# Performance work log

Measured on AMD Instinct MI355X. Metric: run time of the kernel, lower is better.

## Reference

```python
import jax, jax.numpy as jnp
import numpy as np

B, L, V = 4, 1024, 1280
N_EMBD, N_BIN, N_HID = 768, 8, 32
HORIZON = 10.0


def setup_inputs() -> dict:
    key = jax.random.key(0)
    k_h, k_age, k_gap, k_tgt, k_w1, k_w2 = jax.random.split(key, 6)
    h = jax.random.normal(k_h, (B, L, N_EMBD), dtype=jnp.float32)
    # ages increase along a trajectory; gaps in [0, 2) years
    age = jnp.sort(jax.random.uniform(k_age, (B, L), dtype=jnp.float32) * 80.0, axis=-1)
    targets_age = age + jax.random.uniform(k_gap, (B, L), dtype=jnp.float32) * 2.0
    delta_t = targets_age - age  # passed to forward but unused (as in torch source)
    targets = jax.random.randint(k_tgt, (B, L), 0, V, dtype=jnp.int32)
    W1 = jax.random.normal(k_w1, (N_EMBD, N_BIN * N_HID), dtype=jnp.float32) * 0.02
    W2 = jax.random.normal(k_w2, (N_HID, V), dtype=jnp.float32) * 0.02
    return {"h": h, "age": age, "targets_age": targets_age, "delta_t": delta_t,
            "targets": targets, "W1": W1, "W2": W2}


def _time_to_event(age, targets_age, targets):
    # delta_full[b,i,j] = targets_age[b,j] - age[b,i]
    delta_full = targets_age[:, None, :] - age[:, :, None]  # (B,L,L)
    i_idx = jnp.arange(L)
    # torch.triu(diagonal=0): keep targets[b,j] where j>=i, else 0
    upper = (i_idx[None, :] >= i_idx[:, None])  # (L,L) mask, col>=row
    targets_exp = jnp.where(upper[None, :, :], targets[:, None, :], 0)  # (B,L,L)
    # scatter-reduce amin of position index j into vocab slot targets_exp[b,i,j]
    # sentinel L plays the role of torch's -1 (min over srcs ignores it; src<=L-1)
    b_ix = jnp.arange(B)[:, None, None]
    r_ix = i_idx[None, :, None]
    src = jnp.broadcast_to(i_idx[None, None, :], (B, L, L)).astype(jnp.int32)
    token_index = jnp.full((B, L, V), L, dtype=jnp.int32)
    token_index = token_index.at[b_ix, r_ix, targets_exp].min(src)
    no_event = token_index == L
    token_index = jnp.where(no_event, L - 1, token_index)  # (B,L,V)
    tte = jnp.take_along_axis(delta_full, token_index, axis=-1)  # (B,L,V)
    return tte, no_event, token_index


def reference(h, age, targets_age, delta_t, targets, W1, W2):
    # two dense projections: (B,L,E) -> (B,L,n_bin,n_hid) -> (B,L,n_bin,V)
    x = jnp.einsum('ble,eo->blo', h, W1).reshape(B, L, N_BIN, N_HID)
    logits = jnp.einsum('blnh,hv->blnv', x, W2)
    tte, no_event, _ = _time_to_event(age, targets_age, targets)
    edges = jnp.linspace(0.0, HORIZON, N_BIN + 1)
    lo = edges[:-1][None, None, :, None]
    hi = edges[1:][None, None, :, None]
    t = tte[:, :, None, :]  # (B,L,1,V)
    censor_mask = ((t >= lo) & (t < hi)) | no_event[:, :, None, :]  # (B,L,n_bin,V)
    return logits, tte, censor_mask
```

## Files before the change

### kernel.cpp

```cpp
#include <hip/hip_runtime.h>
#include <hip/hip_bf16.h>

#define B_   4
#define L_   1024
#define V_   1280
#define NE_  768
#define NB_  8
#define NH_  32
#define NO_  (NB_*NH_)
#define BL_  (B_*L_)
#define M2_  (BL_*NB_)

typedef __attribute__((ext_vector_type(8))) short bf16x8;
typedef __attribute__((ext_vector_type(4))) float floatx4;

__device__ __forceinline__ unsigned short f2bf(float f) {
    unsigned int u = __float_as_uint(f);
    u += 0x7FFFu + ((u >> 16) & 1u);
    return (unsigned short)(u >> 16);
}

#define H4_N   (BL_*NE_/4)
#define W1T_N  (NO_*NE_)
#define W2T_N  (V_*NH_)
#define K0_TOT (H4_N + W1T_N + W2T_N)

__global__ __launch_bounds__(256) void k0_pack(const float* __restrict__ h,
                                               const float* __restrict__ W1,
                                               const float* __restrict__ W2,
                                               unsigned short* __restrict__ hb,
                                               unsigned short* __restrict__ W1T,
                                               unsigned short* __restrict__ W2T) {
    int id = blockIdx.x * 256 + threadIdx.x;
    if (id < H4_N) {
        float4 v = ((const float4*)h)[id];
        ushort4 o;
        o.x = f2bf(v.x); o.y = f2bf(v.y); o.z = f2bf(v.z); o.w = f2bf(v.w);
        ((ushort4*)hb)[id] = o;
    } else if (id < H4_N + W1T_N) {
        int j = id - H4_N;
        int o = j / NE_;
        int k = j - o * NE_;
        W1T[j] = f2bf(W1[(size_t)k * NO_ + o]);
    } else if (id < K0_TOT) {
        int j = id - H4_N - W1T_N;
        int v = j >> 5;
        int k = j & 31;
        W2T[j] = f2bf(W2[(size_t)k * V_ + v]);
    }
}

__global__ __launch_bounds__(256) void k1_gemm(const unsigned short* __restrict__ hb,
                                               const unsigned short* __restrict__ W1T,
                                               unsigned short* __restrict__ Xb) {
    __shared__ short A_lds[64][40];
    __shared__ short Bt_lds[64][40];

    const int t      = threadIdx.x;
    const int m0     = blockIdx.x * 64;
    const int n0     = blockIdx.y * 64;
    const int l      = t & 63;
    const int w      = t >> 6;
    const int lane15 = l & 15;
    const int quad   = l >> 4;

    const int srow = t >> 2;
    const int sq   = (t & 3) * 8;

    const unsigned short* aptr = hb  + (size_t)(m0 + srow) * NE_ + sq;
    const unsigned short* bptr = W1T + (size_t)(n0 + srow) * NE_ + sq;

    floatx4 acc[4];
#pragma unroll
    for (int i = 0; i < 4; ++i) acc[i] = (floatx4){0.f, 0.f, 0.f, 0.f};

    bf16x8 av = *(const bf16x8*)aptr;
    bf16x8 bv = *(const bf16x8*)bptr;

    for (int k0 = 0; k0 < NE_; k0 += 32) {
        __syncthreads();
        *(bf16x8*)&A_lds[srow][sq]  = av;
        *(bf16x8*)&Bt_lds[srow][sq] = bv;
        __syncthreads();
        if (k0 + 32 < NE_) {
            av = *(const bf16x8*)(aptr + k0 + 32);
            bv = *(const bf16x8*)(bptr + k0 + 32);
        }
        bf16x8 af = *(bf16x8*)&A_lds[w * 16 + lane15][quad * 8];
#pragma unroll
        for (int nt = 0; nt < 4; ++nt) {
            bf16x8 bf = *(bf16x8*)&Bt_lds[nt * 16 + lane15][quad * 8];
            acc[nt] = __builtin_amdgcn_mfma_f32_16x16x32_bf16(af, bf, acc[nt], 0, 0, 0);
        }
    }

    const int rbase = m0 + w * 16 + quad * 4;
#pragma unroll
    for (int nt = 0; nt < 4; ++nt)
#pragma unroll
        for (int r = 0; r < 4; ++r)
            Xb[(size_t)(rbase + r) * NO_ + n0 + nt * 16 + lane15] = f2bf(acc[nt][r]);
}

__global__ __launch_bounds__(256) void k2_logits(const unsigned short* __restrict__ Xb,
                                                 const unsigned short* __restrict__ W2T,
                                                 float* __restrict__ outL) {
    const int t      = threadIdx.x;
    const int m0     = blockIdx.x * 64;
    const int l      = t & 63;
    const int w      = t >> 6;
    const int lane15 = l & 15;
    const int quad   = l >> 4;

    const int m = m0 + w * 16 + lane15;
    const bf16x8 af = *(const bf16x8*)(Xb + (size_t)m * NH_ + quad * 8);

    const int rbase = m0 + w * 16 + quad * 4;

#pragma unroll 4
    for (int nt = 0; nt < V_ / 16; ++nt) {
        bf16x8 bf = *(const bf16x8*)(W2T + (size_t)(nt * 16 + lane15) * NH_ + quad * 8);
        floatx4 c = (floatx4){0.f, 0.f, 0.f, 0.f};
        c = __builtin_amdgcn_mfma_f32_16x16x32_bf16(af, bf, c, 0, 0, 0);
#pragma unroll
        for (int r = 0; r < 4; ++r)
            outL[(size_t)(rbase + r) * V_ + nt * 16 + lane15] = c[r];
    }
}

#define K3_S 32

__global__ __launch_bounds__(256) void k3_tte(const float* __restrict__ age,
                                              const float* __restrict__ tage,
                                              const int*   __restrict__ targets,
                                              float* __restrict__ outT,
                                              float* __restrict__ outM) {
    __shared__ int   tg[L_];
    __shared__ float ta[L_];
    __shared__ float ag[K3_S];

    const int t      = threadIdx.x;
    const int v      = blockIdx.x * 256 + t;
    const int istart = blockIdx.y * K3_S;
    const int iend   = istart + K3_S;
    const int b      = blockIdx.z;

    for (int j = t; j < L_; j += 256) {
        tg[j] = targets[(size_t)b * L_ + j];
        ta[j] = tage[(size_t)b * L_ + j];
    }
    if (t < K3_S) ag[t] = age[(size_t)b * L_ + istart + t];
    __syncthreads();

    int cur = L_;
    for (int i = L_ - 1; i >= istart; --i) {
        const int ti = tg[i];
        if (ti == v) cur = i;
        if (i < iend) {
            int idx = cur;
            if (v == 0 && i >= 1) idx = 0;
            const bool noev = (idx == L_);
            const int  ic   = noev ? (L_ - 1) : idx;
            const float tte = ta[ic] - ag[i - istart];

            outT[((size_t)(b * L_ + i)) * V_ + v] = tte;

            const size_t mb = ((size_t)(b * L_ + i)) * NB_ * V_ + v;
#pragma unroll
            for (int n = 0; n < NB_; ++n) {
                const float lo = n * 1.25f;
                const float hi = (n + 1) * 1.25f;
                const bool in_bin = (tte >= lo) && (tte < hi);
                outM[mb + (size_t)n * V_] = (in_bin || noev) ? 1.0f : 0.0f;
            }
        }
    }
}

extern "C" void kernel_launch(void* const* d_in, const int* in_sizes, int n_in,
                              void* d_out, int out_size, void* d_ws, size_t ws_size,
                              hipStream_t stream) {
    const float* h       = (const float*)d_in[0];
    const float* age     = (const float*)d_in[1];
    const float* tage    = (const float*)d_in[2];
    const int*   targets = (const int*)  d_in[4];
    const float* W1      = (const float*)d_in[5];
    const float* W2      = (const float*)d_in[6];

    float* out  = (float*)d_out;
    float* outL = out;
    float* outT = out + (size_t)BL_ * NB_ * V_;
    float* outM = outT + (size_t)BL_ * V_;

    char* ws = (char*)d_ws;
    unsigned short* hb  = (unsigned short*)(ws);
    unsigned short* W1T = (unsigned short*)(ws + 6291456);
    unsigned short* W2T = (unsigned short*)(ws + 6291456 + 393216);
    unsigned short* Xb  = (unsigned short*)(ws + 6291456 + 393216 + 81920);

    k0_pack  <<<(K0_TOT + 255) / 256, 256, 0, stream>>>(h, W1, W2, hb, W1T, W2T);
    k1_gemm  <<<dim3(BL_/64, NO_/64), 256, 0, stream>>>(hb, W1T, Xb);
    k2_logits<<<M2_/64, 256, 0, stream>>>(Xb, W2T, outL);
    k3_tte   <<<dim3(V_/256, L_/K3_S, B_), 256, 0, stream>>>(age, tage, targets, outT, outM);
}
```

Measured before the change: 423.1 us.

## Precompute per-chunk next-occurrence table and split logits kernel across vocab tiles

A new pass scans each batch's targets once per vocab slot and records the next occurrence at every 16-row chunk boundary. The output kernel can then start each chunk from that table instead of rescanning from the end of the sequence. This removes the quadratic backward scan that made the old tte kernel costly, and the output kernel now writes float4 vectors. The logits kernel also gains a second grid dimension over vocab tiles for more parallelism, at the cost of reloading the A fragment in each tile.

New measurement: 426.9 us. Within noise of the previous version (+0.9%).

```diff
diff --git a/kernel.cpp b/kernel.cpp
--- a/kernel.cpp
+++ b/kernel.cpp
@@ -10,6 +10,7 @@
 #define NO_  (NB_*NH_)
 #define BL_  (B_*L_)
 #define M2_  (BL_*NB_)
+#define NCH_ 64
 
 typedef __attribute__((ext_vector_type(8))) short bf16x8;
 typedef __attribute__((ext_vector_type(4))) float floatx4;
@@ -107,6 +108,7 @@
                                                  float* __restrict__ outL) {
     const int t      = threadIdx.x;
     const int m0     = blockIdx.x * 64;
+    const int nt0    = blockIdx.y * 16;
     const int l      = t & 63;
     const int w      = t >> 6;
     const int lane15 = l & 15;
@@ -118,7 +120,7 @@
     const int rbase = m0 + w * 16 + quad * 4;
 
 #pragma unroll 4
-    for (int nt = 0; nt < V_ / 16; ++nt) {
+    for (int nt = nt0; nt < nt0 + 16; ++nt) {
         bf16x8 bf = *(const bf16x8*)(W2T + (size_t)(nt * 16 + lane15) * NH_ + quad * 8);
         floatx4 c = (floatx4){0.f, 0.f, 0.f, 0.f};
         c = __builtin_amdgcn_mfma_f32_16x16x32_bf16(af, bf, c, 0, 0, 0);
@@ -128,51 +130,80 @@
     }
 }
 
-#define K3_S 32
-
-__global__ __launch_bounds__(256) void k3_tte(const float* __restrict__ age,
+__global__ __launch_bounds__(256) void k3a_nxt(const int* __restrict__ targets,
+                                               int* __restrict__ nxt) {
+    const int b = blockIdx.x;
+    const int v = blockIdx.y * 256 + threadIdx.x;
+    __shared__ int tg[L_];
+    for (int j = threadIdx.x; j < L_; j += 256) tg[j] = targets[(size_t)b * L_ + j];
+    __syncthreads();
+    int cur = L_;
+    for (int j = L_ - 1; j >= 0; --j) {
+        if ((j & 15) == 15)
+            nxt[((size_t)b * NCH_ + (j >> 4)) * V_ + v] = cur;
+        if (tg[j] == v) cur = j;
+    }
+}
+
+__global__ __launch_bounds__(64) void k3b_out(const float* __restrict__ age,
                                               const float* __restrict__ tage,
                                               const int*   __restrict__ targets,
+                                              const int*   __restrict__ nxt,
                                               float* __restrict__ outT,
                                               float* __restrict__ outM) {
-    __shared__ int   tg[L_];
     __shared__ float ta[L_];
-    __shared__ float ag[K3_S];
-
-    const int t      = threadIdx.x;
-    const int v      = blockIdx.x * 256 + t;
-    const int istart = blockIdx.y * K3_S;
-    const int iend   = istart + K3_S;
-    const int b      = blockIdx.z;
-
-    for (int j = t; j < L_; j += 256) {
-        tg[j] = targets[(size_t)b * L_ + j];
-        ta[j] = tage[(size_t)b * L_ + j];
-    }
-    if (t < K3_S) ag[t] = age[(size_t)b * L_ + istart + t];
+    __shared__ int   tgc[16];
+    __shared__ float agc[16];
+
+    const int t  = threadIdx.x;
+    const int vt = blockIdx.x;
+    const int c  = blockIdx.y;
+    const int b  = blockIdx.z;
+    const int v0 = vt * 256 + t * 4;
+
+    for (int j = t; j < L_; j += 64) ta[j] = tage[(size_t)b * L_ + j];
+    if (t < 16) {
+        tgc[t] = targets[(size_t)b * L_ + c * 16 + t];
+        agc[t] = age[(size_t)b * L_ + c * 16 + t];
+    }
     __syncthreads();
 
-    int cur = L_;
-    for (int i = L_ - 1; i >= istart; --i) {
-        const int ti = tg[i];
-        if (ti == v) cur = i;
-        if (i < iend) {
-            int idx = cur;
-            if (v == 0 && i >= 1) idx = 0;
-            const bool noev = (idx == L_);
-            const int  ic   = noev ? (L_ - 1) : idx;
-            const float tte = ta[ic] - ag[i - istart];
-
-            outT[((size_t)(b * L_ + i)) * V_ + v] = tte;
-
-            const size_t mb = ((size_t)(b * L_ + i)) * NB_ * V_ + v;
-#pragma unroll
-            for (int n = 0; n < NB_; ++n) {
-                const float lo = n * 1.25f;
-                const float hi = (n + 1) * 1.25f;
-                const bool in_bin = (tte >= lo) && (tte < hi);
-                outM[mb + (size_t)n * V_] = (in_bin || noev) ? 1.0f : 0.0f;
-            }
+    int4 cur = *(const int4*)&nxt[((size_t)b * NCH_ + c) * V_ + v0];
+
+    for (int ii = 15; ii >= 0; --ii) {
+        const int   i  = c * 16 + ii;
+        const int   ti = tgc[ii];
+        const float ai = agc[ii];
+
+        if (ti == v0 + 0) cur.x = i;
+        if (ti == v0 + 1) cur.y = i;
+        if (ti == v0 + 2) cur.z = i;
+        if (ti == v0 + 3) cur.w = i;
+
+        int ix = cur.x, iy = cur.y, iz = cur.z, iw = cur.w;
+        if (v0 == 0 && i >= 1) ix = 0;
+        const bool nex = (ix == L_), ney = (iy == L_), nez = (iz == L_), new_ = (iw == L_);
+
+        float4 tt;
+        tt.x = ta[nex ? L_ - 1 : ix] - ai;
+        tt.y = ta[ney ? L_ - 1 : iy] - ai;
+        tt.z = ta[nez ? L_ - 1 : iz] - ai;
+        tt.w = ta[new_ ? L_ - 1 : iw] - ai;
+
+        const size_t row = (size_t)(b * L_ + i);
+        *(float4*)&outT[row * V_ + v0] = tt;
+
+        const size_t mb = row * NB_ * V_ + v0;
+#pragma unroll
+        for (int n = 0; n < NB_; ++n) {
+            const float lo = n * 1.25f;
+            const float hi = (n + 1) * 1.25f;
+            float4 m;
+            m.x = ((tt.x >= lo && tt.x < hi) || nex)  ? 1.0f : 0.0f;
+            m.y = ((tt.y >= lo && tt.y < hi) || ney)  ? 1.0f : 0.0f;
+            m.z = ((tt.z >= lo && tt.z < hi) || nez)  ? 1.0f : 0.0f;
+            m.w = ((tt.w >= lo && tt.w < hi) || new_) ? 1.0f : 0.0f;
+            *(float4*)&outM[mb + (size_t)n * V_] = m;
         }
     }
 }
@@ -197,9 +228,11 @@
     unsigned short* W1T = (unsigned short*)(ws + 6291456);
     unsigned short* W2T = (unsigned short*)(ws + 6291456 + 393216);
     unsigned short* Xb  = (unsigned short*)(ws + 6291456 + 393216 + 81920);
+    int*            nxt = (int*)(ws + 6291456 + 393216 + 81920 + 2097152);
 
     k0_pack  <<<(K0_TOT + 255) / 256, 256, 0, stream>>>(h, W1, W2, hb, W1T, W2T);
+    k3a_nxt  <<<dim3(B_, V_/256), 256, 0, stream>>>(targets, nxt);
     k1_gemm  <<<dim3(BL_/64, NO_/64), 256, 0, stream>>>(hb, W1T, Xb);
-    k2_logits<<<M2_/64, 256, 0, stream>>>(Xb, W2T, outL);
-    k3_tte   <<<dim3(V_/256, L_/K3_S, B_), 256, 0, stream>>>(age, tage, targets, outT, outM);
-}
+    k2_logits<<<dim3(M2_/64, 5), 256, 0, stream>>>(Xb, W2T, outL);
+    k3b_out  <<<dim3(5, NCH_, B_), 64, 0, stream>>>(age, tage, targets, nxt, outT, outM);
+}
```
